# Kernel optimization log

Measured on AMD Instinct MI355X. Metric: run time of the kernel, lower is better.

Reference implementation:

```python
import jax, jax.numpy as jnp
import numpy as np

N_NODES = 50000
N_EDGES = 800000
N_GRAPHS = 64
IN_DIM = 128
HID = 128
S, C = 4, 16
DIM1 = 3 * S * S  # 48
OUT_DIM = DIM1 * C  # 768


def gcn_conv(x, W, b, src, dst, w):
    """PyG GCNConv: linear transform, then sym-normalized aggregation with self-loops (weight 1)."""
    n = x.shape[0]
    h = x @ W  # [N, out]
    deg = jnp.zeros((n,), x.dtype).at[dst].add(w) + 1.0  # self-loop weight 1
    dinv = jax.lax.rsqrt(deg)
    norm = dinv[src] * w * dinv[dst]  # [E]
    agg = jnp.zeros_like(h).at[dst].add(h[src] * norm[:, None])
    agg = agg + h * (1.0 / deg)[:, None]  # self-loop messages
    return agg + b


def setup_inputs() -> dict:
    key = jax.random.key(0)
    ks = jax.random.split(key, 16)
    x = jax.random.normal(ks[0], (N_NODES, IN_DIM), jnp.float32)
    edge_index = jax.random.randint(ks[1], (2, N_EDGES), 0, N_NODES, jnp.int64)
    edge_attr = jax.random.uniform(ks[2], (N_EDGES,), jnp.float32)
    batch = jnp.sort(jax.random.randint(ks[3], (N_NODES,), 0, N_GRAPHS, jnp.int64))

    def glorot(k, fan_in, fan_out):
        s = np.sqrt(6.0 / (fan_in + fan_out)).astype(np.float32)
        return jax.random.uniform(k, (fan_in, fan_out), jnp.float32, -s, s)

    return {
        "x": x, "edge_index": edge_index, "edge_attr": edge_attr, "batch": batch,
        "W1": glorot(ks[4], IN_DIM, HID), "b1": jnp.zeros((HID,), jnp.float32),
        "W2": glorot(ks[5], HID, HID // 2), "b2": jnp.zeros((HID // 2,), jnp.float32),
        "W3": glorot(ks[6], HID // 2, HID // 4), "b3": jnp.zeros((HID // 4,), jnp.float32),
        "Wl": glorot(ks[7], HID // 4, OUT_DIM), "bl": jnp.zeros((OUT_DIM,), jnp.float32),
    }


def reference(x, edge_index, edge_attr, batch, W1, b1, W2, b2, W3, b3, Wl, bl):
    src, dst = edge_index[0], edge_index[1]
    w = edge_attr / edge_attr.max()
    h = jax.nn.relu(gcn_conv(x, W1, b1, src, dst, w))
    h = jax.nn.relu(gcn_conv(h, W2, b2, src, dst, w))
    h = jax.nn.relu(gcn_conv(h, W3, b3, src, dst, w))
    # global mean pool over graphs
    sums = jax.ops.segment_sum(h, batch, num_segments=N_GRAPHS)
    cnt = jax.ops.segment_sum(jnp.ones((h.shape[0],), h.dtype), batch, num_segments=N_GRAPHS)
    pooled = sums / jnp.maximum(cnt, 1.0)[:, None]
    out = pooled @ Wl + bl  # [G, OUT_DIM]
    return out.reshape(N_GRAPHS, DIM1, C)
```

## Files before the change

kernel.cpp:

```cpp
#include <hip/hip_runtime.h>
#include <hip/hip_bf16.h>

#define NN 50000
#define NE 800000
#define NG 64
#define OUTD 768

#define G1B ((NN + 63) / 64)
#define SSEG 32
#define TTL 2
#define ESEG (NE / SSEG)
#define NTL (NN / TTL)
#define HRB (SSEG * TTL)

__device__ __forceinline__ float bflo(unsigned int u) { return __uint_as_float(u << 16); }
__device__ __forceinline__ float bfhi(unsigned int u) { return __uint_as_float(u & 0xffff0000u); }
__device__ __forceinline__ unsigned short f2bf(float f) {
    unsigned int u = __float_as_uint(f);
    return (unsigned short)((u + 0x7fffu + ((u >> 16) & 1u)) >> 16);
}
__device__ __forceinline__ unsigned int pack2bf(float lo, float hi) {
    return (unsigned int)f2bf(lo) | ((unsigned int)f2bf(hi) << 16);
}

typedef __attribute__((ext_vector_type(8))) short bf16x8;
typedef __attribute__((ext_vector_type(4))) float f32x4;
union FragU { uint4 u4; bf16x8 v; };

template <int K, int N>
constexpr int mfma_lds_bytes() { return (K / 32) * (N / 16) * 1024; }

template <int K, int N, typename TX>
__device__ __forceinline__ void mfma_gemm_body(char* smem,
                                               const TX* __restrict__ X,
                                               const float* __restrict__ W,
                                               unsigned short* __restrict__ Y,
                                               int nRows, int bx) {
    constexpr int NCT = N / 16;
    constexpr int KS = K / 32;
    const int tid = threadIdx.x;

    for (int q = tid; q < KS * NCT * 64; q += 256) {
        int lane = q & 63;
        int fi = q >> 6;
        int ct = fi % NCT, kc = fi / NCT;
        int col = ct * 16 + (lane & 15);
        int kb = kc * 32 + ((lane >> 4) << 3);
        uint4 w;
        w.x = pack2bf(W[(size_t)(kb + 0) * N + col], W[(size_t)(kb + 1) * N + col]);
        w.y = pack2bf(W[(size_t)(kb + 2) * N + col], W[(size_t)(kb + 3) * N + col]);
        w.z = pack2bf(W[(size_t)(kb + 4) * N + col], W[(size_t)(kb + 5) * N + col]);
        w.w = pack2bf(W[(size_t)(kb + 6) * N + col], W[(size_t)(kb + 7) * N + col]);
        *(uint4*)(smem + (size_t)q * 16) = w;
    }
    __syncthreads();

    const int lane = tid & 63;
    const int wv = tid >> 6;
    const int m = lane & 15;
    const int quad = lane >> 4;
    const int row = bx * 64 + wv * 16 + m;
    const bool rowok = row < nRows;
    const TX* xr = X + (size_t)(rowok ? row : 0) * K;

    f32x4 acc[NCT];
#pragma unroll
    for (int ct = 0; ct < NCT; ++ct) acc[ct] = (f32x4){0.f, 0.f, 0.f, 0.f};

#pragma unroll
    for (int kc = 0; kc < KS; ++kc) {
        const int k0 = kc * 32 + quad * 8;
        FragU a;
        if constexpr (sizeof(TX) == 4) {
            float4 a0 = make_float4(0.f, 0.f, 0.f, 0.f), a1 = a0;
            if (rowok) {
                a0 = *(const float4*)(xr + k0);
                a1 = *(const float4*)(xr + k0 + 4);
            }
            a.u4 = make_uint4(pack2bf(a0.x, a0.y), pack2bf(a0.z, a0.w),
                              pack2bf(a1.x, a1.y), pack2bf(a1.z, a1.w));
        } else {
            a.u4 = rowok ? *(const uint4*)(xr + k0) : make_uint4(0, 0, 0, 0);
        }
#pragma unroll
        for (int ct = 0; ct < NCT; ++ct) {
            FragU b;
            b.u4 = *(const uint4*)(smem + ((size_t)(kc * NCT + ct) * 64 + lane) * 16);
            acc[ct] = __builtin_amdgcn_mfma_f32_16x16x32_bf16(a.v, b.v, acc[ct], 0, 0, 0);
        }
    }

    const int orowb = bx * 64 + wv * 16 + quad * 4;
#pragma unroll
    for (int ct = 0; ct < NCT; ++ct) {
        int col = ct * 16 + m;
#pragma unroll
        for (int r = 0; r < 4; ++r) {
            int orow = orowb + r;
            if (orow < nRows) Y[(size_t)orow * N + col] = f2bf(acc[ct][r]);
        }
    }
}

template <int K, int N, typename TX>
__global__ __launch_bounds__(256) void mfma_gemm_kernel(const TX* __restrict__ X,
                                                        const float* __restrict__ W,
                                                        unsigned short* __restrict__ Y,
                                                        int nRows) {
    extern __shared__ char smem[];
    mfma_gemm_body<K, N>(smem, X, W, Y, nRows, blockIdx.x);
}

__global__ __launch_bounds__(256) void fused1_kernel(const float* __restrict__ x,
                                                     const float* __restrict__ W1,
                                                     unsigned short* __restrict__ bufA,
                                                     const float* __restrict__ ea,
                                                     unsigned int* wmax,
                                                     const int* __restrict__ dst,
                                                     int* __restrict__ rank,
                                                     unsigned short* __restrict__ pcnt) {
    extern __shared__ char smem[];
    const int b = blockIdx.x;
    if (b < G1B) {
        mfma_gemm_body<128, 128>(smem, x, W1, bufA, NN, b);
    } else {
        const int b2 = b - G1B;
        const int seg = b2 >> 1;
        const int tile = b2 & 1;
        unsigned int* lcnt = (unsigned int*)smem;
        float* redm = (float*)(smem + 25600);
        for (int i = threadIdx.x; i < NTL / 4; i += 256) lcnt[i] = 0;
        __syncthreads();
        const int base = seg * ESEG;
        const int nlo = tile * NTL;
        const int4* dst4 = (const int4*)(dst + base);
        const float4* ea4 = (const float4*)(ea + base);
        float m = 0.0f;
        for (int g = threadIdx.x; g < ESEG / 4; g += 256) {
            const int4 v = dst4[g];
            if (tile == 0) {
                const float4 ev = ea4[g];
                m = fmaxf(fmaxf(m, fmaxf(ev.x, ev.y)), fmaxf(ev.z, ev.w));
            }
            const int e0 = base + g * 4;
            const int dd[4] = {v.x, v.y, v.z, v.w};
#pragma unroll
            for (int j = 0; j < 4; ++j) {
                int d = dd[j] - nlo;
                if ((unsigned)d < (unsigned)NTL) {
                    unsigned sh = (unsigned)(d & 3) << 3;
                    unsigned old = atomicAdd(&lcnt[d >> 2], 1u << sh);
                    rank[e0 + j] = (int)((old >> sh) & 0xffu);
                }
            }
        }
        if (tile == 0) {
#pragma unroll
            for (int off = 32; off > 0; off >>= 1) m = fmaxf(m, __shfl_xor(m, off));
            if ((threadIdx.x & 63) == 0) redm[threadIdx.x >> 6] = m;
        }
        __syncthreads();
        unsigned short* prow = pcnt + (size_t)seg * NN + nlo;
        for (int i = threadIdx.x; i < NTL / 4; i += 256) {
            unsigned int w = lcnt[i];
            uint2 o;
            o.x = (w & 0xffu) | ((w & 0xff00u) << 8);
            o.y = ((w >> 16) & 0xffu) | ((w >> 8) & 0xff0000u);
            *(uint2*)(prow + i * 4) = o;
        }
        if (tile == 0 && threadIdx.x == 0) {
            float mm = fmaxf(fmaxf(redm[0], redm[1]), fmaxf(redm[2], redm[3]));
            atomicMax(wmax, __float_as_uint(mm));
        }
    }
}

__global__ __launch_bounds__(256) void comb_kernel(unsigned short* __restrict__ pcnt,
                                                   int* __restrict__ hist,
                                                   int* __restrict__ blocksum) {
    __shared__ int red[256];
    int n = blockIdx.x * 256 + threadIdx.x;
    int run = 0;
    if (n < NN) {
#pragma unroll
        for (int s = 0; s < SSEG; ++s) {
            size_t idx = (size_t)s * NN + n;
            int v = pcnt[idx];
            pcnt[idx] = (unsigned short)run;
            run += v;
        }
        hist[n] = run;
    }
    red[threadIdx.x] = (n < NN) ? run : 0;
    __syncthreads();
    for (int off = 128; off > 0; off >>= 1) {
        if (threadIdx.x < off) red[threadIdx.x] += red[threadIdx.x + off];
        __syncthreads();
    }
    if (threadIdx.x == 0) blocksum[blockIdx.x] = red[0];
}

__global__ __launch_bounds__(256) void scan3_kernel(const int* __restrict__ hist,
                                                    const int* __restrict__ blocksum,
                                                    int* __restrict__ rowptr, int n, int nb) {
    __shared__ int sb[256];
    __shared__ int s[256];
    const int tid = threadIdx.x;
    int bv = (tid < nb) ? blocksum[tid] : 0;
    sb[tid] = bv;
    __syncthreads();
    for (int off = 1; off < 256; off <<= 1) {
        int t = (tid >= off) ? sb[tid - off] : 0;
        __syncthreads();
        sb[tid] += t;
        __syncthreads();
    }
    const int boff = (blockIdx.x > 0) ? sb[blockIdx.x - 1] : 0;
    const int total = sb[nb - 1];

    int i = blockIdx.x * 256 + tid;
    int v = (i < n) ? hist[i] : 0;
    s[tid] = v;
    __syncthreads();
    for (int off = 1; off < 256; off <<= 1) {
        int t = (tid >= off) ? s[tid - off] : 0;
        __syncthreads();
        s[tid] += t;
        __syncthreads();
    }
    if (i < n) rowptr[i] = boff + s[tid] - v;
    if (blockIdx.x == 0 && tid == 0) rowptr[n] = total;
}

__global__ void scat_kernel(const int* __restrict__ src, const int* __restrict__ dst,
                            const float* __restrict__ ea,
                            const int* __restrict__ rowptr,
                            const unsigned short* __restrict__ pcnt,
                            const int* __restrict__ rank,
                            int2* __restrict__ epack, int nE) {
    int e = blockIdx.x * blockDim.x + threadIdx.x;
    if (e >= nE) return;
    int s = e / ESEG;
    int d = dst[e];
    int pos = rowptr[d] + (int)pcnt[(size_t)s * NN + d] + rank[e];
    epack[pos] = make_int2(src[e], __float_as_int(ea[e]));
}

__global__ void deg_kernel(const int2* __restrict__ epack, const int* __restrict__ rowptr,
                           const unsigned int* __restrict__ wmax,
                           float* __restrict__ nrm, float* __restrict__ invdeg, int n) {
    int i = blockIdx.x * blockDim.x + threadIdx.x;
    if (i >= n) return;
    float rw = 1.0f / __uint_as_float(*wmax);
    float srw = sqrtf(rw);
    int s0 = rowptr[i], s1 = rowptr[i + 1];
    float sa = 0.f, sb = 0.f;
    int e = s0;
    for (; e + 2 <= s1; e += 2) {
        sa += __int_as_float(epack[e].y);
        sb += __int_as_float(epack[e + 1].y);
    }
    if (e < s1) sa += __int_as_float(epack[e].y);
    float d = fmaf(sa + sb, rw, 1.0f);
    nrm[i] = rsqrtf(d) * srw;
    invdeg[i] = 1.0f / d;
}

template <int D, bool PRE>
__global__ __launch_bounds__(256) void agg_kernel(const unsigned short* __restrict__ H,
                                                  const int* __restrict__ rowptr,
                                                  int2* __restrict__ epack,
                                                  const float* __restrict__ invdeg,
                                                  const float* __restrict__ nrm,
                                                  const float* __restrict__ bias,
                                                  unsigned short* __restrict__ out,
                                                  int nNodes) {
    constexpr int LPE = D / 8;
    constexpr int EPW = 64 / LPE;
    const int lane = threadIdx.x & 63;
    const int n = (blockIdx.x << 2) | (threadIdx.x >> 6);
    if (n >= nNodes) return;
    const int esub = lane / LPE;
    const int f8 = (lane % LPE) * 8;
    const int s0 = rowptr[n];
    const int cnt = rowptr[n + 1] - s0;
    int2* ep = epack + s0;
    const float dn = PRE ? 1.0f : nrm[n];

    float a[8] = {};
#define AGG8(c_, u_)                                                            \
    a[0] = fmaf(c_, bflo(u_.x), a[0]); a[1] = fmaf(c_, bfhi(u_.x), a[1]);       \
    a[2] = fmaf(c_, bflo(u_.y), a[2]); a[3] = fmaf(c_, bfhi(u_.y), a[3]);       \
    a[4] = fmaf(c_, bflo(u_.z), a[4]); a[5] = fmaf(c_, bfhi(u_.z), a[5]);       \
    a[6] = fmaf(c_, bflo(u_.w), a[6]); a[7] = fmaf(c_, bfhi(u_.w), a[7]);

    int kb = 0;
    for (; kb + 4 * EPW <= cnt; kb += 4 * EPW) {
        const int2 p0 = ep[kb + 0 * EPW + esub];
        const int2 p1 = ep[kb + 1 * EPW + esub];
        const int2 p2 = ep[kb + 2 * EPW + esub];
        const int2 p3 = ep[kb + 3 * EPW + esub];
        const uint4 u0 = *(const uint4*)(H + (size_t)p0.x * D + f8);
        const uint4 u1 = *(const uint4*)(H + (size_t)p1.x * D + f8);
        const uint4 u2 = *(const uint4*)(H + (size_t)p2.x * D + f8);
        const uint4 u3 = *(const uint4*)(H + (size_t)p3.x * D + f8);
        float c0, c1, c2, c3;
        if constexpr (PRE) {
            c0 = __int_as_float(p0.y); c1 = __int_as_float(p1.y);
            c2 = __int_as_float(p2.y); c3 = __int_as_float(p3.y);
        } else {
            c0 = nrm[p0.x] * __int_as_float(p0.y) * dn;
            c1 = nrm[p1.x] * __int_as_float(p1.y) * dn;
            c2 = nrm[p2.x] * __int_as_float(p2.y) * dn;
            c3 = nrm[p3.x] * __int_as_float(p3.y) * dn;
            if (f8 == 0) {
                ep[kb + 0 * EPW + esub].y = __float_as_int(c0);
                ep[kb + 1 * EPW + esub].y = __float_as_int(c1);
                ep[kb + 2 * EPW + esub].y = __float_as_int(c2);
                ep[kb + 3 * EPW + esub].y = __float_as_int(c3);
            }
        }
        AGG8(c0, u0) AGG8(c1, u1) AGG8(c2, u2) AGG8(c3, u3)
    }
    for (; kb + 2 * EPW <= cnt; kb += 2 * EPW) {
        const int2 p0 = ep[kb + esub];
        const int2 p1 = ep[kb + EPW + esub];
        const uint4 u0 = *(const uint4*)(H + (size_t)p0.x * D + f8);
        const uint4 u1 = *(const uint4*)(H + (size_t)p1.x * D + f8);
        float c0, c1;
        if constexpr (PRE) {
            c0 = __int_as_float(p0.y); c1 = __int_as_float(p1.y);
        } else {
            c0 = nrm[p0.x] * __int_as_float(p0.y) * dn;
            c1 = nrm[p1.x] * __int_as_float(p1.y) * dn;
            if (f8 == 0) {
                ep[kb + esub].y = __float_as_int(c0);
                ep[kb + EPW + esub].y = __float_as_int(c1);
            }
        }
        AGG8(c0, u0) AGG8(c1, u1)
    }
    for (; kb < cnt; kb += EPW) {
        const int idx = kb + esub;
        const bool ok = idx < cnt;
        const int2 p = ok ? ep[idx] : make_int2(n, 0);
        const uint4 u = *(const uint4*)(H + (size_t)p.x * D + f8);
        float c;
        if constexpr (PRE) {
            c = ok ? __int_as_float(p.y) : 0.f;
        } else {
            c = ok ? nrm[p.x] * __int_as_float(p.y) * dn : 0.f;
            if (ok && f8 == 0) ep[idx].y = __float_as_int(c);
        }
        AGG8(c, u)
    }
#undef AGG8
#pragma unroll
    for (int off = LPE; off < 64; off <<= 1) {
#pragma unroll
        for (int j = 0; j < 8; ++j) a[j] += __shfl_xor(a[j], off);
    }
    if (esub == 0) {
        const float id = invdeg[n];
        const uint4 un = *(const uint4*)(H + (size_t)n * D + f8);
        const float4 b0 = *(const float4*)(bias + f8);
        const float4 b1 = *(const float4*)(bias + f8 + 4);
        float o[8];
        o[0] = fmaxf(fmaf(id, bflo(un.x), a[0]) + b0.x, 0.f);
        o[1] = fmaxf(fmaf(id, bfhi(un.x), a[1]) + b0.y, 0.f);
        o[2] = fmaxf(fmaf(id, bflo(un.y), a[2]) + b0.z, 0.f);
        o[3] = fmaxf(fmaf(id, bfhi(un.y), a[3]) + b0.w, 0.f);
        o[4] = fmaxf(fmaf(id, bflo(un.z), a[4]) + b1.x, 0.f);
        o[5] = fmaxf(fmaf(id, bfhi(un.z), a[5]) + b1.y, 0.f);
        o[6] = fmaxf(fmaf(id, bflo(un.w), a[6]) + b1.z, 0.f);
        o[7] = fmaxf(fmaf(id, bfhi(un.w), a[7]) + b1.w, 0.f);
        uint4 w;
        w.x = pack2bf(o[0], o[1]);
        w.y = pack2bf(o[2], o[3]);
        w.z = pack2bf(o[4], o[5]);
        w.w = pack2bf(o[6], o[7]);
        *(uint4*)(out + (size_t)n * D + f8) = w;
    }
}

__global__ __launch_bounds__(1024) void poolfin_kernel(const unsigned short* __restrict__ h,
                                                       const int* __restrict__ batch,
                                                       const float* __restrict__ Wl,
                                                       const float* __restrict__ bl,
                                                       float* __restrict__ out, int n) {
    const int g = blockIdx.x;
    int lo = 0, hi = n;
    while (lo < hi) { int m = (lo + hi) >> 1; if (batch[m] < g) lo = m + 1; else hi = m; }
    const int start = lo;
    lo = start; hi = n;
    while (lo < hi) { int m = (lo + hi) >> 1; if (batch[m] < g + 1) lo = m + 1; else hi = m; }
    const int end = lo;

    __shared__ float part[1024];
    __shared__ float spool[32];
    const int f = threadIdx.x & 31;
    const int r = threadIdx.x >> 5;
    float acc = 0.f;
    for (int i = start + r; i < end; i += 32)
        acc += __uint_as_float((unsigned int)h[(size_t)i * 32 + f] << 16);
    part[threadIdx.x] = acc;
    __syncthreads();
    if (threadIdx.x < 32) {
        float s = 0.f;
#pragma unroll
        for (int q = 0; q < 32; ++q) s += part[q * 32 + f];
        float inv = 1.0f / fmaxf((float)(end - start), 1.0f);
        spool[f] = s * inv;
    }
    __syncthreads();
    if (threadIdx.x < OUTD) {
        const int o = threadIdx.x;
        float a2 = bl[o];
#pragma unroll
        for (int k = 0; k < 32; ++k)
            a2 = fmaf(spool[k], Wl[k * OUTD + o], a2);
        out[(size_t)g * OUTD + o] = a2;
    }
}

extern "C" void kernel_launch(void* const* d_in, const int* in_sizes, int n_in,
                              void* d_out, int out_size, void* d_ws, size_t ws_size,
                              hipStream_t stream) {
    const float* x = (const float*)d_in[0];
    const int* eidx = (const int*)d_in[1];
    const float* ea = (const float*)d_in[2];
    const int* batch = (const int*)d_in[3];
    const float* W1 = (const float*)d_in[4];
    const float* b1 = (const float*)d_in[5];
    const float* W2 = (const float*)d_in[6];
    const float* b2 = (const float*)d_in[7];
    const float* W3 = (const float*)d_in[8];
    const float* b3 = (const float*)d_in[9];
    const float* Wl = (const float*)d_in[10];
    const float* bl = (const float*)d_in[11];
    const int* src = eidx;
    const int* dst = eidx + NE;

    char* p = (char*)d_ws;
    auto take = [&](size_t bytes) {
        char* r = p;
        p += (bytes + 255) & ~(size_t)255;
        return r;
    };
    float* nrm = (float*)take(NN * 4);
    float* invdeg = (float*)take(NN * 4);
    int* hist = (int*)take(NN * 4);
    int* rowptr = (int*)take((NN + 1) * 4);
    int* blocksum = (int*)take(256 * 4);
    int2* epack = (int2*)take((size_t)NE * 8);
    unsigned int* wmax = (unsigned int*)take(4);
    unsigned short* bufA = (unsigned short*)take((size_t)NN * 128 * 2);
    unsigned short* bufB = (unsigned short*)take((size_t)NN * 128 * 2);
    int* rank = (int*)bufB;
    unsigned short* pcnt = (unsigned short*)((char*)bufB + (size_t)NE * 4 + 256);

    const int nblk = (NN + 255) / 256;
    const int eblk = (NE + 255) / 256;

    hipMemsetAsync(wmax, 0, 4, stream);

    constexpr int LDS1 = mfma_lds_bytes<128, 128>();
    static_assert(LDS1 >= 25600 + 16, "HR branch LDS (u8 counters + max red) must fit");
    fused1_kernel<<<G1B + HRB, 256, LDS1, stream>>>(x, W1, bufA, ea, wmax,
                                                    dst, rank, pcnt);
    comb_kernel<<<nblk, 256, 0, stream>>>(pcnt, hist, blocksum);
    scan3_kernel<<<nblk, 256, 0, stream>>>(hist, blocksum, rowptr, NN, nblk);
    scat_kernel<<<eblk, 256, 0, stream>>>(src, dst, ea, rowptr, pcnt, rank, epack, NE);
    deg_kernel<<<nblk, 256, 0, stream>>>(epack, rowptr, wmax, nrm, invdeg, NN);

    agg_kernel<128, false><<<(NN + 3) / 4, 256, 0, stream>>>(bufA, rowptr, epack, invdeg, nrm, b1, bufB, NN);
    mfma_gemm_kernel<128, 64, unsigned short>
        <<<G1B, 256, mfma_lds_bytes<128, 64>(), stream>>>(bufB, W2, bufA, NN);
    agg_kernel<64, true><<<(NN + 3) / 4, 256, 0, stream>>>(bufA, rowptr, epack, invdeg, nrm, b2, bufB, NN);
    mfma_gemm_kernel<64, 32, unsigned short>
        <<<G1B, 256, mfma_lds_bytes<64, 32>(), stream>>>(bufB, W3, bufA, NN);
    agg_kernel<32, true><<<(NN + 3) / 4, 256, 0, stream>>>(bufA, rowptr, epack, invdeg, nrm, b3, bufB, NN);

    poolfin_kernel<<<NG, 1024, 0, stream>>>(bufB, batch, Wl, bl, (float*)d_out, NN);
}
```

Measured before the change: 257.1 us.

## Split edge-weight max into dedicated blocks, widen histogram tiles, vectorize scatter

Edge-weight max reduction moves from the tile-0 histogram blocks into 128 dedicated blocks in the fused first kernel. The local-rank histogram now uses 4 node tiles per segment with packed 16-bit LDS counters instead of 2 tiles with 8-bit counters, so the global write becomes a plain copy. The scatter kernel processes 4 edges per thread with vectorized loads. Together these aim to balance the fused kernel's work and cut per-edge instruction and load overhead. The cost is more blocks, each rescanning its segment's dst array for its own tile.

```diff
diff --git a/kernel.cpp b/kernel.cpp
--- a/kernel.cpp
+++ b/kernel.cpp
@@ -7,8 +7,9 @@
 #define OUTD 768
 
 #define G1B ((NN + 63) / 64)
+#define MAXB 128
 #define SSEG 32
-#define TTL 2
+#define TTL 4
 #define ESEG (NE / SSEG)
 #define NTL (NN / TTL)
 #define HRB (SSEG * TTL)
@@ -123,55 +124,50 @@
     const int b = blockIdx.x;
     if (b < G1B) {
         mfma_gemm_body<128, 128>(smem, x, W1, bufA, NN, b);
+    } else if (b < G1B + MAXB) {
+        float* red = (float*)smem;
+        const int bb = b - G1B;
+        const float4* ea4 = (const float4*)ea;
+        float m = 0.0f;
+        for (int i = bb * 256 + threadIdx.x; i < NE / 4; i += MAXB * 256) {
+            float4 v = ea4[i];
+            m = fmaxf(fmaxf(m, fmaxf(v.x, v.y)), fmaxf(v.z, v.w));
+        }
+        red[threadIdx.x] = m;
+        __syncthreads();
+        for (int off = 128; off > 0; off >>= 1) {
+            if (threadIdx.x < off)
+                red[threadIdx.x] = fmaxf(red[threadIdx.x], red[threadIdx.x + off]);
+            __syncthreads();
+        }
+        if (threadIdx.x == 0) atomicMax(wmax, __float_as_uint(red[0]));
     } else {
-        const int b2 = b - G1B;
-        const int seg = b2 >> 1;
-        const int tile = b2 & 1;
+        const int b2 = b - G1B - MAXB;
+        const int seg = b2 >> 2;
+        const int tile = b2 & 3;
         unsigned int* lcnt = (unsigned int*)smem;
-        float* redm = (float*)(smem + 25600);
-        for (int i = threadIdx.x; i < NTL / 4; i += 256) lcnt[i] = 0;
+        for (int i = threadIdx.x; i < NTL / 2; i += 256) lcnt[i] = 0;
         __syncthreads();
         const int base = seg * ESEG;
         const int nlo = tile * NTL;
         const int4* dst4 = (const int4*)(dst + base);
-        const float4* ea4 = (const float4*)(ea + base);
-        float m = 0.0f;
         for (int g = threadIdx.x; g < ESEG / 4; g += 256) {
             const int4 v = dst4[g];
-            if (tile == 0) {
-                const float4 ev = ea4[g];
-                m = fmaxf(fmaxf(m, fmaxf(ev.x, ev.y)), fmaxf(ev.z, ev.w));
-            }
             const int e0 = base + g * 4;
             const int dd[4] = {v.x, v.y, v.z, v.w};
 #pragma unroll
             for (int j = 0; j < 4; ++j) {
                 int d = dd[j] - nlo;
                 if ((unsigned)d < (unsigned)NTL) {
-                    unsigned sh = (unsigned)(d & 3) << 3;
-                    unsigned old = atomicAdd(&lcnt[d >> 2], 1u << sh);
-                    rank[e0 + j] = (int)((old >> sh) & 0xffu);
+                    unsigned sh = (unsigned)(d & 1) << 4;
+                    unsigned old = atomicAdd(&lcnt[d >> 1], 1u << sh);
+                    rank[e0 + j] = (int)((old >> sh) & 0xffffu);
                 }
             }
         }
-        if (tile == 0) {
-#pragma unroll
-            for (int off = 32; off > 0; off >>= 1) m = fmaxf(m, __shfl_xor(m, off));
-            if ((threadIdx.x & 63) == 0) redm[threadIdx.x >> 6] = m;
-        }
-        __syncthreads();
-        unsigned short* prow = pcnt + (size_t)seg * NN + nlo;
-        for (int i = threadIdx.x; i < NTL / 4; i += 256) {
-            unsigned int w = lcnt[i];
-            uint2 o;
-            o.x = (w & 0xffu) | ((w & 0xff00u) << 8);
-            o.y = ((w >> 16) & 0xffu) | ((w >> 8) & 0xff0000u);
-            *(uint2*)(prow + i * 4) = o;
-        }
-        if (tile == 0 && threadIdx.x == 0) {
-            float mm = fmaxf(fmaxf(redm[0], redm[1]), fmaxf(redm[2], redm[3]));
-            atomicMax(wmax, __float_as_uint(mm));
-        }
+        __syncthreads();
+        unsigned int* prow32 = (unsigned int*)(pcnt + (size_t)seg * NN + nlo);
+        for (int i = threadIdx.x; i < NTL / 2; i += 256) prow32[i] = lcnt[i];
     }
 }
 
@@ -237,13 +233,24 @@
                             const int* __restrict__ rowptr,
                             const unsigned short* __restrict__ pcnt,
                             const int* __restrict__ rank,
-                            int2* __restrict__ epack, int nE) {
-    int e = blockIdx.x * blockDim.x + threadIdx.x;
-    if (e >= nE) return;
-    int s = e / ESEG;
-    int d = dst[e];
-    int pos = rowptr[d] + (int)pcnt[(size_t)s * NN + d] + rank[e];
-    epack[pos] = make_int2(src[e], __float_as_int(ea[e]));
+                            int2* __restrict__ epack, int nE4) {
+    int g = blockIdx.x * blockDim.x + threadIdx.x;
+    if (g >= nE4) return;
+    const int s = (g * 4) / ESEG;
+    const size_t pb = (size_t)s * NN;
+    const int4 d4 = ((const int4*)dst)[g];
+    const int4 s4 = ((const int4*)src)[g];
+    const float4 e4 = ((const float4*)ea)[g];
+    const int4 r4 = ((const int4*)rank)[g];
+    const int dd[4] = {d4.x, d4.y, d4.z, d4.w};
+    const int ss[4] = {s4.x, s4.y, s4.z, s4.w};
+    const float ee[4] = {e4.x, e4.y, e4.z, e4.w};
+    const int rr[4] = {r4.x, r4.y, r4.z, r4.w};
+#pragma unroll
+    for (int j = 0; j < 4; ++j) {
+        int pos = rowptr[dd[j]] + (int)pcnt[pb + dd[j]] + rr[j];
+        epack[pos] = make_int2(ss[j], __float_as_int(ee[j]));
+    }
 }
 
 __global__ void deg_kernel(const int2* __restrict__ epack, const int* __restrict__ rowptr,
@@ -460,17 +467,17 @@
     unsigned short* pcnt = (unsigned short*)((char*)bufB + (size_t)NE * 4 + 256);
 
     const int nblk = (NN + 255) / 256;
-    const int eblk = (NE + 255) / 256;
+    const int e4blk = (NE / 4 + 255) / 256;
 
     hipMemsetAsync(wmax, 0, 4, stream);
 
     constexpr int LDS1 = mfma_lds_bytes<128, 128>();
-    static_assert(LDS1 >= 25600 + 16, "HR branch LDS (u8 counters + max red) must fit");
-    fused1_kernel<<<G1B + HRB, 256, LDS1, stream>>>(x, W1, bufA, ea, wmax,
-                                                    dst, rank, pcnt);
+    static_assert(LDS1 >= NTL * 2, "HR branch LDS (packed u16 counters) must fit");
+    fused1_kernel<<<G1B + MAXB + HRB, 256, LDS1, stream>>>(x, W1, bufA, ea, wmax,
+                                                           dst, rank, pcnt);
     comb_kernel<<<nblk, 256, 0, stream>>>(pcnt, hist, blocksum);
     scan3_kernel<<<nblk, 256, 0, stream>>>(hist, blocksum, rowptr, NN, nblk);
-    scat_kernel<<<eblk, 256, 0, stream>>>(src, dst, ea, rowptr, pcnt, rank, epack, NE);
+    scat_kernel<<<e4blk, 256, 0, stream>>>(src, dst, ea, rowptr, pcnt, rank, epack, NE / 4);
     deg_kernel<<<nblk, 256, 0, stream>>>(epack, rowptr, wmax, nrm, invdeg, NN);
 
     agg_kernel<128, false><<<(NN + 3) / 4, 256, 0, stream>>>(bufA, rowptr, epack, invdeg, nrm, b1, bufB, NN);
```

Measured after the change: 261.7 us. No clear change (+1.8%).
